# Kernel optimization log

Measured on AMD Instinct MI355X. Metric: run time of the kernel, lower is better.

Reference implementation:

```python
import jax, jax.numpy as jnp
import numpy as np

ALPHA = 0.2  # leaky_relu negative slope
EPS = 1e-12  # F.normalize eps
N = 8192
E = 262144
DIN = 512
DOUT = 256


def setup_inputs() -> dict:
    key = jax.random.key(0)
    k1, k2, k3, k4, k5 = jax.random.split(key, 5)
    x = jax.random.normal(k1, (N, DIN), dtype=jnp.float32)
    edge_index = jax.random.randint(k2, (2, E), 0, N, dtype=jnp.int64)
    weight = jax.random.normal(k3, (DIN, DOUT), dtype=jnp.float32) * (1.0 / np.sqrt(DIN))
    a = jax.random.normal(k4, (2 * DOUT, 1), dtype=jnp.float32) * (1.0 / np.sqrt(2 * DOUT))
    bias = jnp.zeros((DOUT,), dtype=jnp.float32)
    return {"x": x, "edge_index": edge_index, "weight": weight, "a": a, "bias": bias}


def reference(x, edge_index, weight, a, bias):
    # h: [N, DOUT]
    h = x @ weight
    dout = weight.shape[1]
    # GAT-style additive scores: e[i,j] = leaky_relu(Wh1[i] + Wh2[j])
    Wh1 = h @ a[:dout, :]   # [N, 1]
    Wh2 = h @ a[dout:, :]   # [N, 1]
    e = jax.nn.leaky_relu(Wh1 + Wh2.T, negative_slope=ALPHA)  # [N, N]
    row, col = edge_index[0], edge_index[1]
    # sparse_e.to_dense(): edge entries hold e values (duplicates summed), rest 0
    sparse_dense = jnp.zeros((x.shape[0], x.shape[0]), dtype=e.dtype).at[row, col].add(e[row, col])
    attention = jax.nn.softmax(sparse_dense, axis=1)  # softmax over full dense row incl. zeros
    # dropout is identity in eval mode
    h_pass = attention @ h  # [N, DOUT]
    out = jax.nn.leaky_relu(h_pass, negative_slope=ALPHA)
    norm = jnp.maximum(jnp.linalg.norm(out, ord=2, axis=1, keepdims=True), EPS)
    out = out / norm
    return out + bias
```

## Files before the change

### kernel.cpp

```cpp
#include <hip/hip_runtime.h>

#define NN 8192
#define NE 262144
#define DIN 512
#define DOUT 256
#define LRELU_ALPHA 0.2f
#define RSLOT 96
#define BM 64
#define BN 64
#define BK 64

using bf16x8 = __attribute__((ext_vector_type(8))) short;
using f32x4 = __attribute__((ext_vector_type(4))) float;

__device__ inline unsigned short bf16rne(float f) {
    unsigned u = __float_as_uint(f);
    return (unsigned short)((u + 0x7FFFu + ((u >> 16) & 1u)) >> 16);
}

__device__ inline void split8(const float4 a, const float4 b, bf16x8& hi, bf16x8& lo) {
    unsigned u0 = __float_as_uint(a.x), u1 = __float_as_uint(a.y);
    unsigned u2 = __float_as_uint(a.z), u3 = __float_as_uint(a.w);
    unsigned u4 = __float_as_uint(b.x), u5 = __float_as_uint(b.y);
    unsigned u6 = __float_as_uint(b.z), u7 = __float_as_uint(b.w);
    union { unsigned u[4]; bf16x8 v; } H_, L_;
    H_.u[0] = (u1 & 0xFFFF0000u) | (u0 >> 16);
    H_.u[1] = (u3 & 0xFFFF0000u) | (u2 >> 16);
    H_.u[2] = (u5 & 0xFFFF0000u) | (u4 >> 16);
    H_.u[3] = (u7 & 0xFFFF0000u) | (u6 >> 16);
    float l0 = a.x - __uint_as_float(u0 & 0xFFFF0000u);
    float l1 = a.y - __uint_as_float(u1 & 0xFFFF0000u);
    float l2 = a.z - __uint_as_float(u2 & 0xFFFF0000u);
    float l3 = a.w - __uint_as_float(u3 & 0xFFFF0000u);
    float l4 = b.x - __uint_as_float(u4 & 0xFFFF0000u);
    float l5 = b.y - __uint_as_float(u5 & 0xFFFF0000u);
    float l6 = b.z - __uint_as_float(u6 & 0xFFFF0000u);
    float l7 = b.w - __uint_as_float(u7 & 0xFFFF0000u);
    L_.u[0] = (__float_as_uint(l1) & 0xFFFF0000u) | (__float_as_uint(l0) >> 16);
    L_.u[1] = (__float_as_uint(l3) & 0xFFFF0000u) | (__float_as_uint(l2) >> 16);
    L_.u[2] = (__float_as_uint(l5) & 0xFFFF0000u) | (__float_as_uint(l4) >> 16);
    L_.u[3] = (__float_as_uint(l7) & 0xFFFF0000u) | (__float_as_uint(l6) >> 16);
    hi = H_.v;
    lo = L_.v;
}

__global__ __launch_bounds__(256) void prep_kernel(const float* __restrict__ W,
                                                   const float* __restrict__ X,
                                                   short* __restrict__ Wthi,
                                                   short* __restrict__ Wtlo,
                                                   short* __restrict__ Xhi,
                                                   short* __restrict__ Xlo,
                                                   int* __restrict__ cnt,
                                                   float* __restrict__ Wh1,
                                                   float* __restrict__ Wh2,
                                                   float* __restrict__ Htot) {
    int b = blockIdx.x;
    int t = threadIdx.x;
    if (b < DOUT) {
        int n = b;
        float w0 = W[(size_t)(2 * t) * DOUT + n];
        float w1 = W[(size_t)(2 * t + 1) * DOUT + n];
        unsigned u0 = __float_as_uint(w0), u1 = __float_as_uint(w1);
        unsigned hp = (u1 & 0xFFFF0000u) | (u0 >> 16);
        float l0 = w0 - __uint_as_float(u0 & 0xFFFF0000u);
        float l1 = w1 - __uint_as_float(u1 & 0xFFFF0000u);
        unsigned lp = (__float_as_uint(l1) & 0xFFFF0000u) | (__float_as_uint(l0) >> 16);
        ((unsigned*)Wthi)[n * (DIN / 2) + t] = hp;
        ((unsigned*)Wtlo)[n * (DIN / 2) + t] = lp;
    } else if (b < DOUT + 98) {
        int idx = (b - DOUT) * 256 + t;
        if (idx < NN) cnt[idx] = 0;
        else if (idx < 2 * NN) Wh1[idx - NN] = 0.f;
        else if (idx < 3 * NN) Wh2[idx - 2 * NN] = 0.f;
        else if (idx < 3 * NN + DOUT) Htot[idx - 3 * NN] = 0.f;
    } else {
        size_t base = ((size_t)(b - DOUT - 98) * 256 + t) * 8;
        float4 a = *(const float4*)(X + base);
        float4 c = *(const float4*)(X + base + 4);
        bf16x8 hi, lo;
        split8(a, c, hi, lo);
        *(bf16x8*)(Xhi + base) = hi;
        *(bf16x8*)(Xlo + base) = lo;
    }
}

__device__ inline void stage_tile(const short* __restrict__ src, short* lds, int t) {
#pragma unroll
    for (int j = 0; j < 2; ++j) {
        int sigma = j * 256 + t;
        int row = sigma >> 3;
        int cs = sigma & 7;
        bf16x8 v = *(const bf16x8*)(src + (size_t)row * DIN + cs * 8);
        *(bf16x8*)((char*)lds + row * 128 + (((cs ^ (row & 7))) << 4)) = v;
    }
}

__device__ inline bf16x8 frag_read(const short* lds, int row, int kslot) {
    return *(const bf16x8*)((const char*)lds + row * 128 + ((kslot ^ (row & 7)) << 4));
}

__global__ __launch_bounds__(256) void gemm_edges_kernel(
    const short* __restrict__ Xhi, const short* __restrict__ Xlo,
    const short* __restrict__ Wthi, const short* __restrict__ Wtlo,
    const float* __restrict__ av, const int* __restrict__ ei,
    int* __restrict__ cnt, int* __restrict__ csr_col,
    unsigned short* __restrict__ Hb, float* __restrict__ Wh1,
    float* __restrict__ Wh2, float* __restrict__ Htot) {
    if (blockIdx.x >= 512) {
        int e = (blockIdx.x - 512) * 256 + threadIdx.x;
        int r = ei[e];
        int c = ei[NE + e];
        int slot = atomicAdd(&cnt[r], 1);
        if (slot < RSLOT) csr_col[r * RSLOT + slot] = c;
        return;
    }
    __shared__ short Ah[BM * BK], Al[BM * BK], Bh[BN * BK], Bl[BN * BK];
    int b = blockIdx.x;
    int m0 = (b & 127) * BM;
    int n0b = (b >> 7) * BN;
    int t = threadIdx.x;
    int w = t >> 6, lane = t & 63;
    int wm = w >> 1, wn = w & 1;
    int lr = lane & 15;
    int klg = lane >> 4;
    int m0w = wm * 32;
    int n0w = wn * 32;

    f32x4 acc[2][2] = {};

    for (int k0 = 0; k0 < DIN; k0 += BK) {
        stage_tile(Xhi + (size_t)m0 * DIN + k0, Ah, t);
        stage_tile(Xlo + (size_t)m0 * DIN + k0, Al, t);
        stage_tile(Wthi + (size_t)n0b * DIN + k0, Bh, t);
        stage_tile(Wtlo + (size_t)n0b * DIN + k0, Bl, t);
        __syncthreads();
#pragma unroll
        for (int ksub = 0; ksub < 2; ++ksub) {
            int ks = ksub * 4 + klg;
            bf16x8 ah0 = frag_read(Ah, m0w + lr, ks);
            bf16x8 ah1 = frag_read(Ah, m0w + 16 + lr, ks);
            bf16x8 al0 = frag_read(Al, m0w + lr, ks);
            bf16x8 al1 = frag_read(Al, m0w + 16 + lr, ks);
            bf16x8 bh0 = frag_read(Bh, n0w + lr, ks);
            bf16x8 bh1 = frag_read(Bh, n0w + 16 + lr, ks);
            bf16x8 bl0 = frag_read(Bl, n0w + lr, ks);
            bf16x8 bl1 = frag_read(Bl, n0w + 16 + lr, ks);

            acc[0][0] = __builtin_amdgcn_mfma_f32_16x16x32_bf16(ah0, bh0, acc[0][0], 0, 0, 0);
            acc[0][1] = __builtin_amdgcn_mfma_f32_16x16x32_bf16(ah0, bh1, acc[0][1], 0, 0, 0);
            acc[1][0] = __builtin_amdgcn_mfma_f32_16x16x32_bf16(ah1, bh0, acc[1][0], 0, 0, 0);
            acc[1][1] = __builtin_amdgcn_mfma_f32_16x16x32_bf16(ah1, bh1, acc[1][1], 0, 0, 0);
            acc[0][0] = __builtin_amdgcn_mfma_f32_16x16x32_bf16(ah0, bl0, acc[0][0], 0, 0, 0);
            acc[0][1] = __builtin_amdgcn_mfma_f32_16x16x32_bf16(ah0, bl1, acc[0][1], 0, 0, 0);
            acc[1][0] = __builtin_amdgcn_mfma_f32_16x16x32_bf16(ah1, bl0, acc[1][0], 0, 0, 0);
            acc[1][1] = __builtin_amdgcn_mfma_f32_16x16x32_bf16(ah1, bl1, acc[1][1], 0, 0, 0);
            acc[0][0] = __builtin_amdgcn_mfma_f32_16x16x32_bf16(al0, bh0, acc[0][0], 0, 0, 0);
            acc[0][1] = __builtin_amdgcn_mfma_f32_16x16x32_bf16(al0, bh1, acc[0][1], 0, 0, 0);
            acc[1][0] = __builtin_amdgcn_mfma_f32_16x16x32_bf16(al1, bh0, acc[1][0], 0, 0, 0);
            acc[1][1] = __builtin_amdgcn_mfma_f32_16x16x32_bf16(al1, bh1, acc[1][1], 0, 0, 0);
        }
        __syncthreads();
    }

    int orow = (lane >> 4) * 4;
#pragma unroll
    for (int mt = 0; mt < 2; ++mt)
#pragma unroll
        for (int nt = 0; nt < 2; ++nt)
#pragma unroll
            for (int r = 0; r < 4; ++r)
                Hb[(size_t)(m0 + m0w + mt * 16 + orow + r) * DOUT + n0b + n0w + nt * 16 + lr] =
                    bf16rne(acc[mt][nt][r]);

    float a1v0 = av[n0b + n0w + lr];
    float a1v1 = av[n0b + n0w + 16 + lr];
    float a2v0 = av[DOUT + n0b + n0w + lr];
    float a2v1 = av[DOUT + n0b + n0w + 16 + lr];
#pragma unroll
    for (int mt = 0; mt < 2; ++mt)
#pragma unroll
        for (int r = 0; r < 4; ++r) {
            float d1 = acc[mt][0][r] * a1v0 + acc[mt][1][r] * a1v1;
            float d2 = acc[mt][0][r] * a2v0 + acc[mt][1][r] * a2v1;
#pragma unroll
            for (int ofs = 1; ofs < 16; ofs <<= 1) {
                d1 += __shfl_xor(d1, ofs);
                d2 += __shfl_xor(d2, ofs);
            }
            if (lr == 0) {
                int row = m0 + m0w + mt * 16 + orow + r;
                atomicAdd(&Wh1[row], d1);
                atomicAdd(&Wh2[row], d2);
            }
        }

#pragma unroll
    for (int nt = 0; nt < 2; ++nt) {
        float s = 0.f;
#pragma unroll
        for (int mt = 0; mt < 2; ++mt)
#pragma unroll
            for (int r = 0; r < 4; ++r) s += acc[mt][nt][r];
        s += __shfl_xor(s, 16);
        s += __shfl_xor(s, 32);
        if (lane < 16) atomicAdd(&Htot[n0b + n0w + nt * 16 + lane], s);
    }
}

__global__ __launch_bounds__(256) void row_kernel(
    const unsigned short* __restrict__ Hb, const float* __restrict__ Wh1,
    const float* __restrict__ Wh2, const float* __restrict__ Htot,
    const int* __restrict__ cnt, const int* __restrict__ csr_col,
    const float* __restrict__ bias, float* __restrict__ out) {
    __shared__ int scols[4][RSLOT];
    __shared__ float svv[4][RSLOT];
    int tid = threadIdx.x;
    int w = tid >> 6, lane = tid & 63;
    int i = blockIdx.x * 4 + w;
    int n = cnt[i];
    n = n < RSLOT ? n : RSLOT;
    int* colp = scols[w];
    float* vvp = svv[w];
    for (int t = lane; t < n; t += 64) colp[t] = csr_col[i * RSLOT + t];
    __syncthreads();

    const float NEG_INF = -__builtin_inff();
    float wh1 = Wh1[i];
    float localD = 0.f;
    float localm = 0.f;
    for (int t = lane; t < n; t += 64) {
        int c = colp[t];
        int k = 0;
        bool first = true;
        for (int q = 0; q < n; ++q) {
            int cq = colp[q];
            k += (cq == c);
            if (cq == c && q < t) first = false;
        }
        float v;
        if (first) {
            float s = wh1 + Wh2[c];
            s = s > 0.f ? s : LRELU_ALPHA * s;
            v = (float)k * s;
            localD += 1.f;
            localm = fmaxf(localm, v);
        } else {
            v = NEG_INF;
        }
        vvp[t] = v;
    }

    float m = localm, D = localD;
#pragma unroll
    for (int ofs = 32; ofs > 0; ofs >>= 1) {
        m = fmaxf(m, __shfl_xor(m, ofs));
        D += __shfl_xor(D, ofs);
    }

    float em = expf(-m);
    float localZ = 0.f;
    for (int t = lane; t < n; t += 64) {
        float v = vvp[t];
        if (v != NEG_INF) localZ += expf(v - m);
    }
    float Z = localZ;
#pragma unroll
    for (int ofs = 32; ofs > 0; ofs >>= 1) Z += __shfl_xor(Z, ofs);
    Z += ((float)NN - D) * em;
    float invZ = 1.f / Z;

    for (int t = lane; t < n; t += 64) {
        float v = vvp[t];
        vvp[t] = (v != NEG_INF) ? (expf(v - m) - em) * invZ : 0.f;
    }
    __syncthreads();

    float4 a4[8];
#pragma unroll
    for (int j = 0; j < 8; ++j) a4[j] = make_float4(0.f, 0.f, 0.f, 0.f);
    int t = 0;
    for (; t + 8 <= n; t += 8) {
#pragma unroll
        for (int j = 0; j < 8; ++j) {
            float wc = vvp[t + j];
            int cc = colp[t + j];
            const ushort4 hv = *(const ushort4*)(Hb + (size_t)cc * DOUT + lane * 4);
            a4[j].x = fmaf(wc, __uint_as_float((unsigned)hv.x << 16), a4[j].x);
            a4[j].y = fmaf(wc, __uint_as_float((unsigned)hv.y << 16), a4[j].y);
            a4[j].z = fmaf(wc, __uint_as_float((unsigned)hv.z << 16), a4[j].z);
            a4[j].w = fmaf(wc, __uint_as_float((unsigned)hv.w << 16), a4[j].w);
        }
    }
    for (; t < n; ++t) {
        float wc = vvp[t];
        int cc = colp[t];
        const ushort4 hv = *(const ushort4*)(Hb + (size_t)cc * DOUT + lane * 4);
        a4[0].x = fmaf(wc, __uint_as_float((unsigned)hv.x << 16), a4[0].x);
        a4[0].y = fmaf(wc, __uint_as_float((unsigned)hv.y << 16), a4[0].y);
        a4[0].z = fmaf(wc, __uint_as_float((unsigned)hv.z << 16), a4[0].z);
        a4[0].w = fmaf(wc, __uint_as_float((unsigned)hv.w << 16), a4[0].w);
    }
#pragma unroll
    for (int j = 1; j < 8; ++j) {
        a4[0].x += a4[j].x; a4[0].y += a4[j].y; a4[0].z += a4[j].z; a4[0].w += a4[j].w;
    }
    float bc = em * invZ;
    const float4 ht = *(const float4*)(Htot + lane * 4);
    float4 acc = a4[0];
    acc.x = fmaf(bc, ht.x, acc.x);
    acc.y = fmaf(bc, ht.y, acc.y);
    acc.z = fmaf(bc, ht.z, acc.z);
    acc.w = fmaf(bc, ht.w, acc.w);

    float4 val;
    val.x = acc.x > 0.f ? acc.x : LRELU_ALPHA * acc.x;
    val.y = acc.y > 0.f ? acc.y : LRELU_ALPHA * acc.y;
    val.z = acc.z > 0.f ? acc.z : LRELU_ALPHA * acc.z;
    val.w = acc.w > 0.f ? acc.w : LRELU_ALPHA * acc.w;

    float ssq = val.x * val.x + val.y * val.y + val.z * val.z + val.w * val.w;
#pragma unroll
    for (int ofs = 32; ofs > 0; ofs >>= 1) ssq += __shfl_xor(ssq, ofs);
    float inv_nrm = 1.f / fmaxf(sqrtf(ssq), 1e-12f);

    const float4 b4 = *(const float4*)(bias + lane * 4);
    float4 o;
    o.x = fmaf(val.x, inv_nrm, b4.x);
    o.y = fmaf(val.y, inv_nrm, b4.y);
    o.z = fmaf(val.z, inv_nrm, b4.z);
    o.w = fmaf(val.w, inv_nrm, b4.w);
    *(float4*)(out + (size_t)i * DOUT + lane * 4) = o;
}

extern "C" void kernel_launch(void* const* d_in, const int* in_sizes, int n_in,
                              void* d_out, int out_size, void* d_ws, size_t ws_size,
                              hipStream_t stream) {
    const float* x = (const float*)d_in[0];
    const int* ei = (const int*)d_in[1];
    const float* w = (const float*)d_in[2];
    const float* a = (const float*)d_in[3];
    const float* bias = (const float*)d_in[4];
    float* out = (float*)d_out;

    float* Wh1 = (float*)d_ws;
    float* Wh2 = Wh1 + NN;
    float* Htot = Wh2 + NN;
    int* cnt = (int*)(Htot + DOUT);
    int* csr_col = cnt + NN;
    unsigned short* Hb = (unsigned short*)(csr_col + (size_t)NN * RSLOT);
    short* xhi = (short*)(Hb + (size_t)NN * DOUT);
    short* xlo = xhi + (size_t)NN * DIN;
    short* wthi = xlo + (size_t)NN * DIN;
    short* wtlo = wthi + (size_t)DOUT * DIN;

    prep_kernel<<<DOUT + 98 + (NN * DIN / 2048), 256, 0, stream>>>(
        w, x, wthi, wtlo, xhi, xlo, cnt, Wh1, Wh2, Htot);
    gemm_edges_kernel<<<512 + NE / 256, 256, 0, stream>>>(
        xhi, xlo, wthi, wtlo, a, ei, cnt, csr_col, Hb, Wh1, Wh2, Htot);
    row_kernel<<<NN / 4, 256, 0, stream>>>(Hb, Wh1, Wh2, Htot, cnt, csr_col, bias, out);
}
```

Before: 58.40 us.

## Fuse X bf16 hi/lo split into GEMM staging with register prefetch

Removes the separate pass in the prep kernel that split X into bf16 hi/lo arrays in global memory. The GEMM now loads fp32 X tiles directly, splits them in registers while writing to LDS, and prefetches the next k-tile of X and W into registers after the barrier so the global loads overlap the MFMA work. This avoids writing and re-reading 16 MB of split data, at the cost of doing the split redundantly in each of the 4 N-column blocks and using more registers.

```diff
diff --git a/kernel.cpp b/kernel.cpp
--- a/kernel.cpp
+++ b/kernel.cpp
@@ -45,11 +45,8 @@
 }
 
 __global__ __launch_bounds__(256) void prep_kernel(const float* __restrict__ W,
-                                                   const float* __restrict__ X,
                                                    short* __restrict__ Wthi,
                                                    short* __restrict__ Wtlo,
-                                                   short* __restrict__ Xhi,
-                                                   short* __restrict__ Xlo,
                                                    int* __restrict__ cnt,
                                                    float* __restrict__ Wh1,
                                                    float* __restrict__ Wh2,
@@ -67,31 +64,12 @@
         unsigned lp = (__float_as_uint(l1) & 0xFFFF0000u) | (__float_as_uint(l0) >> 16);
         ((unsigned*)Wthi)[n * (DIN / 2) + t] = hp;
         ((unsigned*)Wtlo)[n * (DIN / 2) + t] = lp;
-    } else if (b < DOUT + 98) {
+    } else {
         int idx = (b - DOUT) * 256 + t;
         if (idx < NN) cnt[idx] = 0;
         else if (idx < 2 * NN) Wh1[idx - NN] = 0.f;
         else if (idx < 3 * NN) Wh2[idx - 2 * NN] = 0.f;
         else if (idx < 3 * NN + DOUT) Htot[idx - 3 * NN] = 0.f;
-    } else {
-        size_t base = ((size_t)(b - DOUT - 98) * 256 + t) * 8;
-        float4 a = *(const float4*)(X + base);
-        float4 c = *(const float4*)(X + base + 4);
-        bf16x8 hi, lo;
-        split8(a, c, hi, lo);
-        *(bf16x8*)(Xhi + base) = hi;
-        *(bf16x8*)(Xlo + base) = lo;
-    }
-}
-
-__device__ inline void stage_tile(const short* __restrict__ src, short* lds, int t) {
-#pragma unroll
-    for (int j = 0; j < 2; ++j) {
-        int sigma = j * 256 + t;
-        int row = sigma >> 3;
-        int cs = sigma & 7;
-        bf16x8 v = *(const bf16x8*)(src + (size_t)row * DIN + cs * 8);
-        *(bf16x8*)((char*)lds + row * 128 + (((cs ^ (row & 7))) << 4)) = v;
     }
 }
 
@@ -100,7 +78,7 @@
 }
 
 __global__ __launch_bounds__(256) void gemm_edges_kernel(
-    const short* __restrict__ Xhi, const short* __restrict__ Xlo,
+    const float* __restrict__ X,
     const short* __restrict__ Wthi, const short* __restrict__ Wtlo,
     const float* __restrict__ av, const int* __restrict__ ei,
     int* __restrict__ cnt, int* __restrict__ csr_col,
@@ -126,14 +104,50 @@
     int m0w = wm * 32;
     int n0w = wn * 32;
 
+    int srow0 = t >> 3;
+    int scs = t & 7;
+
     f32x4 acc[2][2] = {};
+    float4 px[2][2];
+    bf16x8 pbh[2], pbl[2];
+
+#pragma unroll
+    for (int j = 0; j < 2; ++j) {
+        int row = j * 32 + srow0;
+        const float* xs = X + (size_t)(m0 + row) * DIN + scs * 8;
+        px[j][0] = *(const float4*)xs;
+        px[j][1] = *(const float4*)(xs + 4);
+        pbh[j] = *(const bf16x8*)(Wthi + (size_t)(n0b + row) * DIN + scs * 8);
+        pbl[j] = *(const bf16x8*)(Wtlo + (size_t)(n0b + row) * DIN + scs * 8);
+    }
 
     for (int k0 = 0; k0 < DIN; k0 += BK) {
-        stage_tile(Xhi + (size_t)m0 * DIN + k0, Ah, t);
-        stage_tile(Xlo + (size_t)m0 * DIN + k0, Al, t);
-        stage_tile(Wthi + (size_t)n0b * DIN + k0, Bh, t);
-        stage_tile(Wtlo + (size_t)n0b * DIN + k0, Bl, t);
+#pragma unroll
+        for (int j = 0; j < 2; ++j) {
+            int row = j * 32 + srow0;
+            int so = ((scs ^ (row & 7)) << 4);
+            bf16x8 hi, lo;
+            split8(px[j][0], px[j][1], hi, lo);
+            *(bf16x8*)((char*)Ah + row * 128 + so) = hi;
+            *(bf16x8*)((char*)Al + row * 128 + so) = lo;
+            *(bf16x8*)((char*)Bh + row * 128 + so) = pbh[j];
+            *(bf16x8*)((char*)Bl + row * 128 + so) = pbl[j];
+        }
         __syncthreads();
+
+        int kn = k0 + BK;
+        if (kn < DIN) {
+#pragma unroll
+            for (int j = 0; j < 2; ++j) {
+                int row = j * 32 + srow0;
+                const float* xs = X + (size_t)(m0 + row) * DIN + kn + scs * 8;
+                px[j][0] = *(const float4*)xs;
+                px[j][1] = *(const float4*)(xs + 4);
+                pbh[j] = *(const bf16x8*)(Wthi + (size_t)(n0b + row) * DIN + kn + scs * 8);
+                pbl[j] = *(const bf16x8*)(Wtlo + (size_t)(n0b + row) * DIN + kn + scs * 8);
+            }
+        }
+
 #pragma unroll
         for (int ksub = 0; ksub < 2; ++ksub) {
             int ks = ksub * 4 + klg;
@@ -348,14 +362,11 @@
     int* cnt = (int*)(Htot + DOUT);
     int* csr_col = cnt + NN;
     unsigned short* Hb = (unsigned short*)(csr_col + (size_t)NN * RSLOT);
-    short* xhi = (short*)(Hb + (size_t)NN * DOUT);
-    short* xlo = xhi + (size_t)NN * DIN;
-    short* wthi = xlo + (size_t)NN * DIN;
+    short* wthi = (short*)(Hb + (size_t)NN * DOUT);
     short* wtlo = wthi + (size_t)DOUT * DIN;
 
-    prep_kernel<<<DOUT + 98 + (NN * DIN / 2048), 256, 0, stream>>>(
-        w, x, wthi, wtlo, xhi, xlo, cnt, Wh1, Wh2, Htot);
+    prep_kernel<<<DOUT + 98, 256, 0, stream>>>(w, wthi, wtlo, cnt, Wh1, Wh2, Htot);
     gemm_edges_kernel<<<512 + NE / 256, 256, 0, stream>>>(
-        xhi, xlo, wthi, wtlo, a, ei, cnt, csr_col, Hb, Wh1, Wh2, Htot);
+        x, wthi, wtlo, a, ei, cnt, csr_col, Hb, Wh1, Wh2, Htot);
     row_kernel<<<NN / 4, 256, 0, stream>>>(Hb, Wh1, Wh2, Htot, cnt, csr_col, bias, out);
 }
```

Result: no change. 57.84 us, median of 2 (-1.0%).
